# Optimization experiments

Measured on AMD Instinct MI355X. Metric: run time of the kernel, lower is better.

## Reference

```python
import jax, jax.numpy as jnp
import numpy as np

B, L, H, E = 4, 2048, 8, 64
NEG = -1e30  # stand-in for the repo's -3.4e38 overflow-to-inf masking trick


def setup_inputs() -> dict:
    key = jax.random.key(0)
    kq, kk, kv = jax.random.split(key, 3)
    return {
        "queries": jax.random.normal(kq, (B, L, H, E), dtype=jnp.float32),
        "keys": jax.random.normal(kk, (B, L, H, E), dtype=jnp.float32),
        "values": jax.random.normal(kv, (B, L, H, E), dtype=jnp.float32),
    }


def reference(queries, keys, values):
    b, l, h, e = queries.shape
    s = keys.shape[1]
    scale = 1.0 / np.sqrt(e).astype(np.float32)
    # [B,H,L,S] scores, materialized as in the original einsum
    scores = jnp.einsum('blhe,bshe->bhls', queries, keys)
    causal = jnp.tril(jnp.ones((l, s), dtype=bool))  # True = visible
    scores = jnp.where(causal, scores, NEG)
    A = jax.nn.softmax(scale * scores, axis=-1)  # dropout is identity at inference
    return jnp.einsum('bhls,bshd->blhd', A, values)
```

## Files before the change

### kernel.cpp

```cpp
#include <hip/hip_runtime.h>
#include <hip/hip_bf16.h>

namespace {

constexpr int B_ = 4, L = 2048, H = 8, E = 64;
constexpr int RS = H * E;
constexpr float CS = 0.125f * 1.44269504f;
constexpr float THR2 = 11.5f;

constexpr size_t ACCF = (size_t)2 * 32 * 8 * 128 * 64;
constexpr size_t MOFF = ACCF;
constexpr size_t PART_ROWS = (size_t)32 * 8 * 128;
constexpr size_t LOFF = MOFF + 2 * PART_ROWS;
constexpr size_t PART_FLOATS = LOFF + 2 * PART_ROWS;

typedef __attribute__((ext_vector_type(8))) short bf16x8;
typedef __attribute__((ext_vector_type(4))) float f32x4;

__device__ inline unsigned cvt2(float a, float b) {
  __hip_bfloat162 hh = __float22bfloat162_rn(make_float2(a, b));
  union { __hip_bfloat162 h; unsigned u; } c; c.h = hh; return c.u;
}

__global__ __launch_bounds__(512)
void fa_split(const float* __restrict__ Q, const float* __restrict__ K,
              const float* __restrict__ V, float* __restrict__ O,
              float* __restrict__ ws, int splitMode)
{
  const int tid  = (int)threadIdx.x;
  const int lane = tid & 63;
  const int wv   = tid >> 6;
  const int bi   = (int)blockIdx.x;
  const int bh   = bi & 31;
  const int pp   = (bi >> 5) & 7;
  const int role = splitMode ? (bi >> 8) : 2;
  const int b = bh >> 3, h = bh & 7;
  const int ln = lane & 15, lg = lane >> 4, d0 = lg * 4;

  int total, ph1sb0, qgA, k0A, qgB; bool finA, finB; int part;
  const int g = pp, v = 15 - pp;
  if (role == 0)      { total = 17; ph1sb0 = 2*g+2; qgA = g; k0A = 0;        finA = true;  qgB = v; finB = false; part = 0; }
  else if (role == 1) { total = 17; ph1sb0 = 1000;  qgA = v; k0A = 15 - 2*g; finA = false; qgB = 0; finB = false; part = 1; }
  else                { total = 34; ph1sb0 = 2*g+2; qgA = g; k0A = 0;        finA = true;  qgB = v; finB = true;  part = 0; }

  const size_t base = (size_t)b * L * RS + (size_t)h * E;
  const float* Qb = Q + base;
  const float* Kb = K + base;
  const float* Vb = V + base;
  float*       Ob = O + base;

  __shared__ __align__(16) unsigned char KT[2][64 * 128];
  __shared__ __align__(16) unsigned char VT[2][64 * 128];

  const int vdd = tid & 63, vc = tid >> 6;
  const int vkb = 4 * vc + ((vc >> 2) << 4);
  const int kky = tid >> 3, kc = tid & 7;
  float vr[8]; float4 kr0, kr1;

  auto stage_load = [&](int ks) {
    const int kv0 = ks * 64;
    const float* vp = Vb + (size_t)(kv0 + vkb) * RS + vdd;
#pragma unroll
    for (int j = 0; j < 4; ++j) vr[j] = vp[(size_t)j * RS];
#pragma unroll
    for (int j = 0; j < 4; ++j) vr[4 + j] = vp[(size_t)(16 + j) * RS];
    const float* kp = Kb + (size_t)(kv0 + kky) * RS + 8 * kc;
    kr0 = *(const float4*)kp; kr1 = *(const float4*)(kp + 4);
  };
  auto stage_write = [&](int bufI) {
    union { uint4 q; unsigned u[4]; } w;
    w.u[0] = cvt2(vr[0], vr[1]); w.u[1] = cvt2(vr[2], vr[3]);
    w.u[2] = cvt2(vr[4], vr[5]); w.u[3] = cvt2(vr[6], vr[7]);
    *(uint4*)(VT[bufI] + vdd * 128 + 16 * (vc ^ (vdd & 7))) = w.q;
    union { uint4 q; unsigned u[4]; } y;
    y.u[0] = cvt2(kr0.x, kr0.y); y.u[1] = cvt2(kr0.z, kr0.w);
    y.u[2] = cvt2(kr1.x, kr1.y); y.u[3] = cvt2(kr1.z, kr1.w);
    *(uint4*)(KT[bufI] + kky * 128 + 16 * (kc ^ (kky & 7))) = y.q;
  };

  int qg = qgA; bool curFin = finA;
  int qrow0 = qg * 128 + wv * 16;
  int nsW   = (qrow0 + 79) >> 6;

  bf16x8 qf0, qf1;
  auto load_q = [&]() {
    const float* qp = Qb + (size_t)(qrow0 + ln) * RS + 8 * lg;
    float4 a = *(const float4*)qp,        c = *(const float4*)(qp + 4);
    float4 d = *(const float4*)(qp + 32), e = *(const float4*)(qp + 36);
    union { bf16x8 v8; unsigned u[4]; } r0, r1;
    r0.u[0] = cvt2(a.x * CS, a.y * CS); r0.u[1] = cvt2(a.z * CS, a.w * CS);
    r0.u[2] = cvt2(c.x * CS, c.y * CS); r0.u[3] = cvt2(c.z * CS, c.w * CS);
    r1.u[0] = cvt2(d.x * CS, d.y * CS); r1.u[1] = cvt2(d.z * CS, d.w * CS);
    r1.u[2] = cvt2(e.x * CS, e.y * CS); r1.u[3] = cvt2(e.z * CS, e.w * CS);
    qf0 = r0.v8; qf1 = r1.v8;
  };
  load_q();

  f32x4 acc[4];
#pragma unroll
  for (int nt = 0; nt < 4; ++nt) acc[nt] = (f32x4){0.f, 0.f, 0.f, 0.f};
  float m = -1e30f, lsum = 0.f;

  auto epilogue = [&]() {
    float ls = lsum + __shfl_xor(lsum, 16, 64);
    ls += __shfl_xor(ls, 32, 64);
    if (curFin) {
      const float il = 1.0f / ls;
      float inv[4];
#pragma unroll
      for (int r = 0; r < 4; ++r) inv[r] = __shfl(il, d0 + r, 64);
#pragma unroll
      for (int nt = 0; nt < 4; ++nt)
#pragma unroll
        for (int r = 0; r < 4; ++r)
          Ob[(size_t)(qrow0 + d0 + r) * RS + (ln + 16 * nt)] = acc[nt][r] * inv[r];
    } else {
      const int vg = qg - 8;
      const size_t rb = ((size_t)part * 32 + bh) * 1024 + (size_t)vg * 128;
#pragma unroll
      for (int nt = 0; nt < 4; ++nt)
#pragma unroll
        for (int r = 0; r < 4; ++r)
          ws[(rb + wv * 16 + d0 + r) * 64 + ln + 16 * nt] = acc[nt][r];
      if (lane < 16) {
        ws[MOFF + rb + wv * 16 + lane] = m;
        ws[LOFF + rb + wv * 16 + lane] = ls;
      }
    }
  };

  stage_load(k0A);
  stage_write(0);
  __syncthreads();
  int buf = 0;

  for (int sb = 0; sb < total; ++sb) {
    const bool haveNext = (sb + 1) < total;
    if (haveNext) {
      const int sn = sb + 1;
      stage_load((sn < ph1sb0) ? (k0A + sn) : (sn - ph1sb0));
    }
    const int kstep = (sb < ph1sb0) ? (k0A + sb) : (sb - ph1sb0);

    if (kstep < nsW) {
      const unsigned char* Kt = KT[buf];
      const int swzr = 16 * (ln & 7);

      f32x4 st[4];
#pragma unroll
      for (int kt = 0; kt < 4; ++kt) {
        const unsigned char* kr = Kt + (16 * kt + ln) * 128;
        const bf16x8 kfa = *(const bf16x8*)(kr + ((16 * lg) ^ swzr));
        const bf16x8 kfb = *(const bf16x8*)(kr + ((16 * lg + 64) ^ swzr));
        f32x4 s = (f32x4){0.f, 0.f, 0.f, 0.f};
        s = __builtin_amdgcn_mfma_f32_16x16x32_bf16(kfa, qf0, s, 0, 0, 0);
        s = __builtin_amdgcn_mfma_f32_16x16x32_bf16(kfb, qf1, s, 0, 0, 0);
        st[kt] = s;
      }

      float x[16];
#pragma unroll
      for (int kt = 0; kt < 4; ++kt)
#pragma unroll
        for (int r = 0; r < 4; ++r) x[4 * kt + r] = st[kt][r];

      if (kstep == nsW - 1) {
        const int kv0 = kstep * 64;
        const int qr = qrow0 + ln;
#pragma unroll
        for (int kt = 0; kt < 4; ++kt)
#pragma unroll
          for (int r = 0; r < 4; ++r) {
            const int key = kv0 + 16 * kt + d0 + r;
            if (key > qr) x[4 * kt + r] = -1e30f;
          }
      }

      float t8[8];
#pragma unroll
      for (int e = 0; e < 8; ++e) t8[e] = fmaxf(x[e], x[8 + e]);
      float t4a = fmaxf(t8[0], t8[4]), t4b = fmaxf(t8[1], t8[5]);
      float t4c = fmaxf(t8[2], t8[6]), t4d = fmaxf(t8[3], t8[7]);
      float mx = fmaxf(fmaxf(t4a, t4b), fmaxf(t4c, t4d));

      if (!__all(mx <= m + THR2)) {
        float gm = fmaxf(mx, __shfl_xor(mx, 16, 64));
        gm = fmaxf(gm, __shfl_xor(gm, 32, 64));
        const float newm = fmaxf(m, gm);
        const float sc = __builtin_exp2f(m - newm);
        lsum *= sc;
        float scr[4];
#pragma unroll
        for (int r = 0; r < 4; ++r) scr[r] = __shfl(sc, d0 + r, 64);
#pragma unroll
        for (int nt = 0; nt < 4; ++nt) {
          acc[nt][0] *= scr[0]; acc[nt][1] *= scr[1];
          acc[nt][2] *= scr[2]; acc[nt][3] *= scr[3];
        }
        m = newm;
      }

      float p[16];
#pragma unroll
      for (int e = 0; e < 16; ++e) p[e] = __builtin_exp2f(x[e] - m);
      {
        float s8[8];
#pragma unroll
        for (int e = 0; e < 8; ++e) s8[e] = p[e] + p[8 + e];
        float s4a = s8[0] + s8[4], s4b = s8[1] + s8[5];
        float s4c = s8[2] + s8[6], s4d = s8[3] + s8[7];
        lsum += (s4a + s4b) + (s4c + s4d);
      }

      const unsigned char* Vt = VT[buf];
#pragma unroll
      for (int kg = 0; kg < 2; ++kg) {
        union { bf16x8 v8; unsigned u[4]; } pf;
#pragma unroll
        for (int j = 0; j < 4; ++j)
          pf.u[j] = cvt2(p[8 * kg + 2 * j], p[8 * kg + 2 * j + 1]);
#pragma unroll
        for (int nt = 0; nt < 4; ++nt) {
          const int row = ln + 16 * nt;
          const bf16x8 vf = *(const bf16x8*)(
              Vt + row * 128 + 16 * ((lg + 4 * kg) ^ (ln & 7)));
          acc[nt] = __builtin_amdgcn_mfma_f32_16x16x32_bf16(pf.v8, vf, acc[nt], 0, 0, 0);
        }
      }
    }

    if (sb == ph1sb0 - 1) {
      epilogue();
#pragma unroll
      for (int nt = 0; nt < 4; ++nt) acc[nt] = (f32x4){0.f, 0.f, 0.f, 0.f};
      m = -1e30f; lsum = 0.f;
      qg = qgB; curFin = finB;
      qrow0 = qg * 128 + wv * 16;
      nsW = (qrow0 + 79) >> 6;
      load_q();
    }

    if (haveNext) stage_write(buf ^ 1);
    __syncthreads();
    buf ^= 1;
  }

  epilogue();
}

__global__ __launch_bounds__(256)
void fa_merge(const float* __restrict__ ws, float* __restrict__ O)
{
  const int idx = (int)blockIdx.x * 256 + (int)threadIdx.x;
  const int d4  = idx & 15;
  const int row = (idx >> 4) & 127;
  const int vg  = (idx >> 11) & 7;
  const int bh  = idx >> 14;
  const size_t rbase = ((size_t)bh * 8 + vg) * 128 + row;

  const float m0 = ws[MOFF + rbase],             l0 = ws[LOFF + rbase];
  const float m1 = ws[MOFF + PART_ROWS + rbase], l1 = ws[LOFF + PART_ROWS + rbase];
  const float M  = fmaxf(m0, m1);
  const float e0 = __builtin_exp2f(m0 - M), e1 = __builtin_exp2f(m1 - M);
  const float inv = 1.0f / (l0 * e0 + l1 * e1);

  const float4 a0 = *(const float4*)(ws + rbase * 64 + 4 * d4);
  const float4 a1 = *(const float4*)(ws + PART_ROWS * 64 + rbase * 64 + 4 * d4);

  const int b = bh >> 3, h = bh & 7;
  const int orow = (8 + vg) * 128 + row;
  float4 o;
  o.x = (a0.x * e0 + a1.x * e1) * inv;
  o.y = (a0.y * e0 + a1.y * e1) * inv;
  o.z = (a0.z * e0 + a1.z * e1) * inv;
  o.w = (a0.w * e0 + a1.w * e1) * inv;
  *(float4*)(O + ((size_t)(b * L + orow) * H + h) * E + 4 * d4) = o;
}

}

extern "C" void kernel_launch(void* const* d_in, const int* in_sizes, int n_in,
                              void* d_out, int out_size, void* d_ws, size_t ws_size,
                              hipStream_t stream) {
  const float* Q = (const float*)d_in[0];
  const float* K = (const float*)d_in[1];
  const float* V = (const float*)d_in[2];
  float* O = (float*)d_out;
  (void)in_sizes; (void)n_in; (void)out_size;

  const bool split = ws_size >= PART_FLOATS * sizeof(float);
  if (split) {
    fa_split<<<512, 512, 0, stream>>>(Q, K, V, O, (float*)d_ws, 1);
    fa_merge<<<2048, 256, 0, stream>>>((const float*)d_ws, O);
  } else {
    fa_split<<<256, 512, 0, stream>>>(Q, K, V, O, (float*)d_ws, 0);
  }
}
```

Measured before the change: 53.14 us.

## Split causal attention work into finer KV chunks with bf16 partial accumulators

Replaces the two-phase paired-query-group schedule with 1024 blocks, each handling a single query group over a KV range. Heavy groups are split into three or four KV chunks, so each block does about the same amount of work on the 256 CUs. Partial accumulators are stored as bf16 in the MFMA fragment layout to halve workspace traffic, and a table-driven merge kernel combines two or three partials per group. This costs an extra bf16 rounding of partial outputs and more merge work and launches.

```diff
diff --git a/kernel.cpp b/kernel.cpp
--- a/kernel.cpp
+++ b/kernel.cpp
@@ -8,11 +8,11 @@
 constexpr float CS = 0.125f * 1.44269504f;
 constexpr float THR2 = 11.5f;
 
-constexpr size_t ACCF = (size_t)2 * 32 * 8 * 128 * 64;
-constexpr size_t MOFF = ACCF;
-constexpr size_t PART_ROWS = (size_t)32 * 8 * 128;
-constexpr size_t LOFF = MOFF + 2 * PART_ROWS;
-constexpr size_t PART_FLOATS = LOFF + 2 * PART_ROWS;
+constexpr size_t ACC_UINTS = (size_t)4 * 32 * 8 * 4096;
+constexpr size_t MOFF = ACC_UINTS;
+constexpr size_t MCNT = (size_t)4 * 32 * 8 * 128;
+constexpr size_t LOFF = MOFF + MCNT;
+constexpr size_t WS_FLOATS = LOFF + MCNT;
 
 typedef __attribute__((ext_vector_type(8))) short bf16x8;
 typedef __attribute__((ext_vector_type(4))) float f32x4;
@@ -20,6 +20,9 @@
 __device__ inline unsigned cvt2(float a, float b) {
   __hip_bfloat162 hh = __float22bfloat162_rn(make_float2(a, b));
   union { __hip_bfloat162 h; unsigned u; } c; c.h = hh; return c.u;
+}
+__device__ inline float bf2f(unsigned short u) {
+  union { unsigned u; float f; } c; c.u = (unsigned)u << 16; return c.f;
 }
 
 __global__ __launch_bounds__(512)
@@ -33,15 +36,36 @@
   const int bi   = (int)blockIdx.x;
   const int bh   = bi & 31;
   const int pp   = (bi >> 5) & 7;
-  const int role = splitMode ? (bi >> 8) : 2;
+  const int role = bi >> 8;
   const int b = bh >> 3, h = bh & 7;
   const int ln = lane & 15, lg = lane >> 4, d0 = lg * 4;
 
-  int total, ph1sb0, qgA, k0A, qgB; bool finA, finB; int part;
   const int g = pp, v = 15 - pp;
-  if (role == 0)      { total = 17; ph1sb0 = 2*g+2; qgA = g; k0A = 0;        finA = true;  qgB = v; finB = false; part = 0; }
-  else if (role == 1) { total = 17; ph1sb0 = 1000;  qgA = v; k0A = 15 - 2*g; finA = false; qgB = 0; finB = false; part = 1; }
-  else                { total = 34; ph1sb0 = 2*g+2; qgA = g; k0A = 0;        finA = true;  qgB = v; finB = true;  part = 0; }
+  const int b0 = 2 * g + 2, nsv = 32 - 2 * g;
+
+  int grp, kLo, kHi, slot = -1; bool fin = false;
+  if (splitMode) {
+    if (g <= 4) {
+      if (role == 0) { grp = g; kLo = 0; kHi = b0; fin = true; }
+      else {
+        const int c1 = (nsv + 2) / 3, c2 = c1 + (nsv - c1 + 1) / 2;
+        grp = v; slot = role;
+        if (role == 1)      { kLo = 0;  kHi = c1; }
+        else if (role == 2) { kLo = c1; kHi = c2; }
+        else                { kLo = c2; kHi = nsv; }
+      }
+    } else {
+      const int hh = b0 / 2, hv = nsv / 2;
+      if (role == 0)      { grp = g; kLo = 0;  kHi = hh;  slot = 0; }
+      else if (role == 1) { grp = g; kLo = hh; kHi = b0;  slot = 1; }
+      else if (role == 2) { grp = v; kLo = 0;  kHi = hv;  slot = 2; }
+      else                { grp = v; kLo = hv; kHi = nsv; slot = 3; }
+    }
+  } else {
+    if (role == 0) { grp = g; kLo = 0; kHi = b0; }
+    else           { grp = v; kLo = 0; kHi = nsv; }
+    fin = true;
+  }
 
   const size_t base = (size_t)b * L * RS + (size_t)h * E;
   const float* Qb = Q + base;
@@ -78,12 +102,11 @@
     *(uint4*)(KT[bufI] + kky * 128 + 16 * (kc ^ (kky & 7))) = y.q;
   };
 
-  int qg = qgA; bool curFin = finA;
-  int qrow0 = qg * 128 + wv * 16;
-  int nsW   = (qrow0 + 79) >> 6;
+  const int qrow0 = grp * 128 + wv * 16;
+  const int nsW   = (qrow0 + 79) >> 6;
 
   bf16x8 qf0, qf1;
-  auto load_q = [&]() {
+  {
     const float* qp = Qb + (size_t)(qrow0 + ln) * RS + 8 * lg;
     float4 a = *(const float4*)qp,        c = *(const float4*)(qp + 4);
     float4 d = *(const float4*)(qp + 32), e = *(const float4*)(qp + 36);
@@ -93,56 +116,23 @@
     r1.u[0] = cvt2(d.x * CS, d.y * CS); r1.u[1] = cvt2(d.z * CS, d.w * CS);
     r1.u[2] = cvt2(e.x * CS, e.y * CS); r1.u[3] = cvt2(e.z * CS, e.w * CS);
     qf0 = r0.v8; qf1 = r1.v8;
-  };
-  load_q();
+  }
 
   f32x4 acc[4];
 #pragma unroll
   for (int nt = 0; nt < 4; ++nt) acc[nt] = (f32x4){0.f, 0.f, 0.f, 0.f};
   float m = -1e30f, lsum = 0.f;
 
-  auto epilogue = [&]() {
-    float ls = lsum + __shfl_xor(lsum, 16, 64);
-    ls += __shfl_xor(ls, 32, 64);
-    if (curFin) {
-      const float il = 1.0f / ls;
-      float inv[4];
-#pragma unroll
-      for (int r = 0; r < 4; ++r) inv[r] = __shfl(il, d0 + r, 64);
-#pragma unroll
-      for (int nt = 0; nt < 4; ++nt)
-#pragma unroll
-        for (int r = 0; r < 4; ++r)
-          Ob[(size_t)(qrow0 + d0 + r) * RS + (ln + 16 * nt)] = acc[nt][r] * inv[r];
-    } else {
-      const int vg = qg - 8;
-      const size_t rb = ((size_t)part * 32 + bh) * 1024 + (size_t)vg * 128;
-#pragma unroll
-      for (int nt = 0; nt < 4; ++nt)
-#pragma unroll
-        for (int r = 0; r < 4; ++r)
-          ws[(rb + wv * 16 + d0 + r) * 64 + ln + 16 * nt] = acc[nt][r];
-      if (lane < 16) {
-        ws[MOFF + rb + wv * 16 + lane] = m;
-        ws[LOFF + rb + wv * 16 + lane] = ls;
-      }
-    }
-  };
-
-  stage_load(k0A);
+  stage_load(kLo);
   stage_write(0);
   __syncthreads();
   int buf = 0;
 
-  for (int sb = 0; sb < total; ++sb) {
-    const bool haveNext = (sb + 1) < total;
-    if (haveNext) {
-      const int sn = sb + 1;
-      stage_load((sn < ph1sb0) ? (k0A + sn) : (sn - ph1sb0));
-    }
-    const int kstep = (sb < ph1sb0) ? (k0A + sb) : (sb - ph1sb0);
-
-    if (kstep < nsW) {
+  for (int ks = kLo; ks < kHi; ++ks) {
+    const bool haveNext = (ks + 1) < kHi;
+    if (haveNext) stage_load(ks + 1);
+
+    if (ks < nsW) {
       const unsigned char* Kt = KT[buf];
       const int swzr = 16 * (ln & 7);
 
@@ -164,8 +154,8 @@
 #pragma unroll
         for (int r = 0; r < 4; ++r) x[4 * kt + r] = st[kt][r];
 
-      if (kstep == nsW - 1) {
-        const int kv0 = kstep * 64;
+      if (ks == nsW - 1) {
+        const int kv0 = ks * 64;
         const int qr = qrow0 + ln;
 #pragma unroll
         for (int kt = 0; kt < 4; ++kt)
@@ -229,52 +219,103 @@
       }
     }
 
-    if (sb == ph1sb0 - 1) {
-      epilogue();
-#pragma unroll
-      for (int nt = 0; nt < 4; ++nt) acc[nt] = (f32x4){0.f, 0.f, 0.f, 0.f};
-      m = -1e30f; lsum = 0.f;
-      qg = qgB; curFin = finB;
-      qrow0 = qg * 128 + wv * 16;
-      nsW = (qrow0 + 79) >> 6;
-      load_q();
-    }
-
     if (haveNext) stage_write(buf ^ 1);
     __syncthreads();
     buf ^= 1;
   }
 
-  epilogue();
+  float ls = lsum + __shfl_xor(lsum, 16, 64);
+  ls += __shfl_xor(ls, 32, 64);
+  if (fin) {
+    const float il = 1.0f / ls;
+    float inv[4];
+#pragma unroll
+    for (int r = 0; r < 4; ++r) inv[r] = __shfl(il, d0 + r, 64);
+#pragma unroll
+    for (int nt = 0; nt < 4; ++nt)
+#pragma unroll
+      for (int r = 0; r < 4; ++r)
+        Ob[(size_t)(qrow0 + d0 + r) * RS + (ln + 16 * nt)] = acc[nt][r] * inv[r];
+  } else {
+    unsigned* wsu = (unsigned*)ws;
+    const size_t ubase =
+        ((((size_t)slot * 32 + bh) * 8 + pp) * 8 + wv) * 512 + (size_t)lane * 8;
+    uint4 u0, u1;
+    u0.x = cvt2(acc[0][0], acc[0][1]); u0.y = cvt2(acc[0][2], acc[0][3]);
+    u0.z = cvt2(acc[1][0], acc[1][1]); u0.w = cvt2(acc[1][2], acc[1][3]);
+    u1.x = cvt2(acc[2][0], acc[2][1]); u1.y = cvt2(acc[2][2], acc[2][3]);
+    u1.z = cvt2(acc[3][0], acc[3][1]); u1.w = cvt2(acc[3][2], acc[3][3]);
+    *(uint4*)(wsu + ubase)     = u0;
+    *(uint4*)(wsu + ubase + 4) = u1;
+    if (lane < 16) {
+      const size_t mi = (((size_t)slot * 32 + bh) * 8 + pp) * 128 + wv * 16 + lane;
+      ws[MOFF + mi] = m;
+      ws[LOFF + mi] = ls;
+    }
+  }
 }
 
 __global__ __launch_bounds__(256)
 void fa_merge(const float* __restrict__ ws, float* __restrict__ O)
 {
-  const int idx = (int)blockIdx.x * 256 + (int)threadIdx.x;
-  const int d4  = idx & 15;
-  const int row = (idx >> 4) & 127;
-  const int vg  = (idx >> 11) & 7;
-  const int bh  = idx >> 14;
-  const size_t rbase = ((size_t)bh * 8 + vg) * 128 + row;
-
-  const float m0 = ws[MOFF + rbase],             l0 = ws[LOFF + rbase];
-  const float m1 = ws[MOFF + PART_ROWS + rbase], l1 = ws[LOFF + PART_ROWS + rbase];
-  const float M  = fmaxf(m0, m1);
-  const float e0 = __builtin_exp2f(m0 - M), e1 = __builtin_exp2f(m1 - M);
-  const float inv = 1.0f / (l0 * e0 + l1 * e1);
-
-  const float4 a0 = *(const float4*)(ws + rbase * 64 + 4 * d4);
-  const float4 a1 = *(const float4*)(ws + PART_ROWS * 64 + rbase * 64 + 4 * d4);
+  const int bi  = (int)blockIdx.x;
+  const int sub = bi & 7;
+  const int pr  = bi >> 3;
+  const int gi  = pr >> 5, bh = pr & 31;
+  const int tid = (int)threadIdx.x;
+  const int d4  = tid & 15;
+  const int row = sub * 16 + (tid >> 4);
+
+  const int Gt[11] = {5,6,7, 8,9,10, 11,12,13,14,15};
+  const int nS[11] = {2,2,2, 2,2,2, 3,3,3,3,3};
+  const int S0[11] = {0,0,0, 2,2,2, 1,1,1,1,1};
+  const int S1[11] = {1,1,1, 3,3,3, 2,2,2,2,2};
+  const int S2[11] = {0,0,0, 0,0,0, 3,3,3,3,3};
+
+  const int G  = Gt[gi];
+  const int n  = nS[gi];
+  const int pp = (G <= 7) ? G : (15 - G);
+  int sl[3] = {S0[gi], S1[gi], S2[gi]};
+
+  float mv[3], lv[3];
+#pragma unroll
+  for (int i = 0; i < 3; ++i) {
+    if (i < n) {
+      const size_t mi = (((size_t)sl[i] * 32 + bh) * 8 + pp) * 128 + row;
+      mv[i] = ws[MOFF + mi]; lv[i] = ws[LOFF + mi];
+    } else { mv[i] = -1e30f; lv[i] = 0.f; }
+  }
+  float M = fmaxf(mv[0], mv[1]); if (n > 2) M = fmaxf(M, mv[2]);
+  float w[3]; float den = 0.f;
+#pragma unroll
+  for (int i = 0; i < 3; ++i) {
+    w[i] = (i < n) ? __builtin_exp2f(mv[i] - M) : 0.f;
+    den += lv[i] * w[i];
+  }
+  const float inv = 1.0f / den;
+
+  const int wvq = row >> 4, lgq = (row & 15) >> 2, r = row & 3;
+  const int rp = r >> 1, rlo = r & 1;
+  const unsigned short* wsh = (const unsigned short*)ws;
+  float o[4] = {0.f, 0.f, 0.f, 0.f};
+#pragma unroll
+  for (int i = 0; i < 3; ++i) {
+    if (i >= n) break;
+    const size_t base_u =
+        ((((size_t)sl[i] * 32 + bh) * 8 + pp) * 8 + wvq) * 512;
+#pragma unroll
+    for (int j = 0; j < 4; ++j) {
+      const int dim = 4 * d4 + j;
+      const int ln = dim & 15, nt = dim >> 4;
+      const size_t ua = base_u + (size_t)(lgq * 16 + ln) * 8 + nt * 2 + rp;
+      o[j] += bf2f(wsh[ua * 2 + rlo]) * w[i];
+    }
+  }
 
   const int b = bh >> 3, h = bh & 7;
-  const int orow = (8 + vg) * 128 + row;
-  float4 o;
-  o.x = (a0.x * e0 + a1.x * e1) * inv;
-  o.y = (a0.y * e0 + a1.y * e1) * inv;
-  o.z = (a0.z * e0 + a1.z * e1) * inv;
-  o.w = (a0.w * e0 + a1.w * e1) * inv;
-  *(float4*)(O + ((size_t)(b * L + orow) * H + h) * E + 4 * d4) = o;
+  const size_t off = ((size_t)(b * L + G * 128 + row) * H + h) * E + 4 * d4;
+  float4 ov; ov.x = o[0] * inv; ov.y = o[1] * inv; ov.z = o[2] * inv; ov.w = o[3] * inv;
+  *(float4*)(O + off) = ov;
 }
 
 }
@@ -288,11 +329,11 @@
   float* O = (float*)d_out;
   (void)in_sizes; (void)n_in; (void)out_size;
 
-  const bool split = ws_size >= PART_FLOATS * sizeof(float);
+  const bool split = ws_size >= WS_FLOATS * sizeof(float);
   if (split) {
-    fa_split<<<512, 512, 0, stream>>>(Q, K, V, O, (float*)d_ws, 1);
-    fa_merge<<<2048, 256, 0, stream>>>((const float*)d_ws, O);
+    fa_split<<<1024, 512, 0, stream>>>(Q, K, V, O, (float*)d_ws, 1);
+    fa_merge<<<2816, 256, 0, stream>>>((const float*)d_ws, O);
   } else {
-    fa_split<<<256, 512, 0, stream>>>(Q, K, V, O, (float*)d_ws, 0);
-  }
-}
+    fa_split<<<512, 512, 0, stream>>>(Q, K, V, O, (float*)d_ws, 0);
+  }
+}
```

Measured after the change: 64.30 us. +21.0%, slower.

## Switch to 32x32x16 MFMA with 32-row waves and 256-row query groups

Applied to the files above, without the earlier changes.

Replaces the 16x16x32 bf16 MFMA tiles with 32x32x16 tiles so each wave handles 32 query rows, and makes each block cover 256 query rows, halving the grid. The split schedule is rebuilt around 8 query groups, with 18 steps per role. P is rearranged into the MFMA A-operand layout using v_permlane32_swap, avoiding a trip through LDS. This aims to reuse K/V tiles loaded into LDS across more rows and to issue fewer MFMA instructions, at the cost of higher register pressure and only 256 blocks on a chip with 256 CUs, which may leave occupancy low.

```diff
diff --git a/kernel.cpp b/kernel.cpp
--- a/kernel.cpp
+++ b/kernel.cpp
@@ -14,8 +14,8 @@
 constexpr size_t LOFF = MOFF + 2 * PART_ROWS;
 constexpr size_t PART_FLOATS = LOFF + 2 * PART_ROWS;
 
-typedef __attribute__((ext_vector_type(8))) short bf16x8;
-typedef __attribute__((ext_vector_type(4))) float f32x4;
+typedef __attribute__((ext_vector_type(8)))  short bf16x8;
+typedef __attribute__((ext_vector_type(16))) float f32x16;
 
 __device__ inline unsigned cvt2(float a, float b) {
   __hip_bfloat162 hh = __float22bfloat162_rn(make_float2(a, b));
@@ -32,16 +32,22 @@
   const int wv   = tid >> 6;
   const int bi   = (int)blockIdx.x;
   const int bh   = bi & 31;
-  const int pp   = (bi >> 5) & 7;
-  const int role = splitMode ? (bi >> 8) : 2;
+  const int pq   = (bi >> 5) & 3;
+  const int role = splitMode ? (bi >> 7) : 0;
   const int b = bh >> 3, h = bh & 7;
-  const int ln = lane & 15, lg = lane >> 4, d0 = lg * 4;
-
-  int total, ph1sb0, qgA, k0A, qgB; bool finA, finB; int part;
-  const int g = pp, v = 15 - pp;
-  if (role == 0)      { total = 17; ph1sb0 = 2*g+2; qgA = g; k0A = 0;        finA = true;  qgB = v; finB = false; part = 0; }
-  else if (role == 1) { total = 17; ph1sb0 = 1000;  qgA = v; k0A = 15 - 2*g; finA = false; qgB = 0; finB = false; part = 1; }
-  else                { total = 34; ph1sb0 = 2*g+2; qgA = g; k0A = 0;        finA = true;  qgB = v; finB = true;  part = 0; }
+  const int ln32 = lane & 31, hb = lane >> 5;
+  const int rsw  = ln32 & 7;
+
+  const int g = pq, v = 7 - pq;
+  const int ng = 4 * g + 4;
+
+  int total, ph1, grpA, k0A, grpB; bool finA, finB; int part;
+  if (splitMode) {
+    if (role == 0) { total = 18; ph1 = ng;   grpA = g; k0A = 0;       finA = true;  grpB = v; finB = false; part = 0; }
+    else           { total = 18; ph1 = 1000; grpA = v; k0A = 18 - ng; finA = false; grpB = 0; finB = false; part = 1; }
+  } else {
+    total = 36; ph1 = ng; grpA = g; k0A = 0; finA = true; grpB = v; finB = true; part = 0;
+  }
 
   const size_t base = (size_t)b * L * RS + (size_t)h * E;
   const float* Qb = Q + base;
@@ -53,17 +59,14 @@
   __shared__ __align__(16) unsigned char VT[2][64 * 128];
 
   const int vdd = tid & 63, vc = tid >> 6;
-  const int vkb = 4 * vc + ((vc >> 2) << 4);
   const int kky = tid >> 3, kc = tid & 7;
   float vr[8]; float4 kr0, kr1;
 
   auto stage_load = [&](int ks) {
     const int kv0 = ks * 64;
-    const float* vp = Vb + (size_t)(kv0 + vkb) * RS + vdd;
-#pragma unroll
-    for (int j = 0; j < 4; ++j) vr[j] = vp[(size_t)j * RS];
-#pragma unroll
-    for (int j = 0; j < 4; ++j) vr[4 + j] = vp[(size_t)(16 + j) * RS];
+    const float* vp = Vb + (size_t)(kv0 + 8 * vc) * RS + vdd;
+#pragma unroll
+    for (int j = 0; j < 8; ++j) vr[j] = vp[(size_t)j * RS];
     const float* kp = Kb + (size_t)(kv0 + kky) * RS + 8 * kc;
     kr0 = *(const float4*)kp; kr1 = *(const float4*)(kp + 4);
   };
@@ -78,53 +81,54 @@
     *(uint4*)(KT[bufI] + kky * 128 + 16 * (kc ^ (kky & 7))) = y.q;
   };
 
-  int qg = qgA; bool curFin = finA;
-  int qrow0 = qg * 128 + wv * 16;
-  int nsW   = (qrow0 + 79) >> 6;
-
-  bf16x8 qf0, qf1;
+  int grp = grpA; bool curFin = finA;
+  int qrow0 = grp * 256 + wv * 32;
+  int nsW   = 4 * grp + 1 + (wv >> 1);
+
+  bf16x8 qf[4];
   auto load_q = [&]() {
-    const float* qp = Qb + (size_t)(qrow0 + ln) * RS + 8 * lg;
-    float4 a = *(const float4*)qp,        c = *(const float4*)(qp + 4);
-    float4 d = *(const float4*)(qp + 32), e = *(const float4*)(qp + 36);
-    union { bf16x8 v8; unsigned u[4]; } r0, r1;
-    r0.u[0] = cvt2(a.x * CS, a.y * CS); r0.u[1] = cvt2(a.z * CS, a.w * CS);
-    r0.u[2] = cvt2(c.x * CS, c.y * CS); r0.u[3] = cvt2(c.z * CS, c.w * CS);
-    r1.u[0] = cvt2(d.x * CS, d.y * CS); r1.u[1] = cvt2(d.z * CS, d.w * CS);
-    r1.u[2] = cvt2(e.x * CS, e.y * CS); r1.u[3] = cvt2(e.z * CS, e.w * CS);
-    qf0 = r0.v8; qf1 = r1.v8;
+    const float* qp = Qb + (size_t)(qrow0 + ln32) * RS + 8 * hb;
+#pragma unroll
+    for (int ds = 0; ds < 4; ++ds) {
+      float4 a = *(const float4*)(qp + 16 * ds);
+      float4 c = *(const float4*)(qp + 16 * ds + 4);
+      union { bf16x8 v8; unsigned u[4]; } r;
+      r.u[0] = cvt2(a.x * CS, a.y * CS); r.u[1] = cvt2(a.z * CS, a.w * CS);
+      r.u[2] = cvt2(c.x * CS, c.y * CS); r.u[3] = cvt2(c.z * CS, c.w * CS);
+      qf[ds] = r.v8;
+    }
   };
   load_q();
 
-  f32x4 acc[4];
-#pragma unroll
-  for (int nt = 0; nt < 4; ++nt) acc[nt] = (f32x4){0.f, 0.f, 0.f, 0.f};
+  f32x16 zero;
+#pragma unroll
+  for (int i = 0; i < 16; ++i) zero[i] = 0.f;
+  f32x16 accA = zero, accB = zero;
   float m = -1e30f, lsum = 0.f;
 
   auto epilogue = [&]() {
-    float ls = lsum + __shfl_xor(lsum, 16, 64);
-    ls += __shfl_xor(ls, 32, 64);
+    float ls = lsum + __shfl_xor(lsum, 32, 64);
     if (curFin) {
       const float il = 1.0f / ls;
-      float inv[4];
-#pragma unroll
-      for (int r = 0; r < 4; ++r) inv[r] = __shfl(il, d0 + r, 64);
-#pragma unroll
-      for (int nt = 0; nt < 4; ++nt)
-#pragma unroll
-        for (int r = 0; r < 4; ++r)
-          Ob[(size_t)(qrow0 + d0 + r) * RS + (ln + 16 * nt)] = acc[nt][r] * inv[r];
+#pragma unroll
+      for (int r2 = 0; r2 < 16; ++r2) {
+        const int row = (r2 & 3) + 8 * (r2 >> 2) + 4 * hb;
+        const float inv = __shfl(il, row, 64);
+        Ob[(size_t)(qrow0 + row) * RS + ln32]      = accA[r2] * inv;
+        Ob[(size_t)(qrow0 + row) * RS + 32 + ln32] = accB[r2] * inv;
+      }
     } else {
-      const int vg = qg - 8;
-      const size_t rb = ((size_t)part * 32 + bh) * 1024 + (size_t)vg * 128;
-#pragma unroll
-      for (int nt = 0; nt < 4; ++nt)
-#pragma unroll
-        for (int r = 0; r < 4; ++r)
-          ws[(rb + wv * 16 + d0 + r) * 64 + ln + 16 * nt] = acc[nt][r];
-      if (lane < 16) {
-        ws[MOFF + rb + wv * 16 + lane] = m;
-        ws[LOFF + rb + wv * 16 + lane] = ls;
+      const size_t rb = ((size_t)part * 32 + bh) * 1024 + (size_t)(grp - 4) * 256;
+#pragma unroll
+      for (int r2 = 0; r2 < 16; ++r2) {
+        const int row = (r2 & 3) + 8 * (r2 >> 2) + 4 * hb;
+        const size_t lr = rb + wv * 32 + row;
+        ws[lr * 64 + ln32]      = accA[r2];
+        ws[lr * 64 + 32 + ln32] = accB[r2];
+      }
+      if (lane < 32) {
+        ws[MOFF + rb + wv * 32 + lane] = m;
+        ws[LOFF + rb + wv * 32 + lane] = ls;
       }
     }
   };
@@ -138,105 +142,109 @@
     const bool haveNext = (sb + 1) < total;
     if (haveNext) {
       const int sn = sb + 1;
-      stage_load((sn < ph1sb0) ? (k0A + sn) : (sn - ph1sb0));
-    }
-    const int kstep = (sb < ph1sb0) ? (k0A + sb) : (sb - ph1sb0);
+      stage_load((sn < ph1) ? (k0A + sn) : (sn - ph1));
+    }
+    const int kstep = (sb < ph1) ? (k0A + sb) : (sb - ph1);
 
     if (kstep < nsW) {
       const unsigned char* Kt = KT[buf];
-      const int swzr = 16 * (ln & 7);
-
-      f32x4 st[4];
-#pragma unroll
-      for (int kt = 0; kt < 4; ++kt) {
-        const unsigned char* kr = Kt + (16 * kt + ln) * 128;
-        const bf16x8 kfa = *(const bf16x8*)(kr + ((16 * lg) ^ swzr));
-        const bf16x8 kfb = *(const bf16x8*)(kr + ((16 * lg + 64) ^ swzr));
-        f32x4 s = (f32x4){0.f, 0.f, 0.f, 0.f};
-        s = __builtin_amdgcn_mfma_f32_16x16x32_bf16(kfa, qf0, s, 0, 0, 0);
-        s = __builtin_amdgcn_mfma_f32_16x16x32_bf16(kfb, qf1, s, 0, 0, 0);
-        st[kt] = s;
-      }
-
-      float x[16];
-#pragma unroll
-      for (int kt = 0; kt < 4; ++kt)
-#pragma unroll
-        for (int r = 0; r < 4; ++r) x[4 * kt + r] = st[kt][r];
+
+      f32x16 st0 = zero, st1 = zero;
+#pragma unroll
+      for (int ds = 0; ds < 4; ++ds) {
+        const int ch = 16 * ((2 * ds + hb) ^ rsw);
+        const bf16x8 kf0 = *(const bf16x8*)(Kt + ln32 * 128 + ch);
+        const bf16x8 kf1 = *(const bf16x8*)(Kt + (32 + ln32) * 128 + ch);
+        st0 = __builtin_amdgcn_mfma_f32_32x32x16_bf16(kf0, qf[ds], st0, 0, 0, 0);
+        st1 = __builtin_amdgcn_mfma_f32_32x32x16_bf16(kf1, qf[ds], st1, 0, 0, 0);
+      }
+
+      float x[32];
+#pragma unroll
+      for (int r2 = 0; r2 < 16; ++r2) { x[r2] = st0[r2]; x[16 + r2] = st1[r2]; }
 
       if (kstep == nsW - 1) {
         const int kv0 = kstep * 64;
-        const int qr = qrow0 + ln;
-#pragma unroll
-        for (int kt = 0; kt < 4; ++kt)
-#pragma unroll
-          for (int r = 0; r < 4; ++r) {
-            const int key = kv0 + 16 * kt + d0 + r;
-            if (key > qr) x[4 * kt + r] = -1e30f;
-          }
-      }
-
+        const int qr = qrow0 + ln32;
+#pragma unroll
+        for (int e = 0; e < 32; ++e) {
+          const int key = kv0 + 32 * (e >> 4) + 8 * ((e >> 2) & 3) + (e & 3) + 4 * hb;
+          if (key > qr) x[e] = -1e30f;
+        }
+      }
+
+      float t16[16];
+#pragma unroll
+      for (int e = 0; e < 16; ++e) t16[e] = fmaxf(x[e], x[16 + e]);
       float t8[8];
 #pragma unroll
-      for (int e = 0; e < 8; ++e) t8[e] = fmaxf(x[e], x[8 + e]);
+      for (int e = 0; e < 8; ++e) t8[e] = fmaxf(t16[e], t16[8 + e]);
       float t4a = fmaxf(t8[0], t8[4]), t4b = fmaxf(t8[1], t8[5]);
       float t4c = fmaxf(t8[2], t8[6]), t4d = fmaxf(t8[3], t8[7]);
-      float mx = fmaxf(fmaxf(t4a, t4b), fmaxf(t4c, t4d));
+      const float mx = fmaxf(fmaxf(t4a, t4b), fmaxf(t4c, t4d));
 
       if (!__all(mx <= m + THR2)) {
-        float gm = fmaxf(mx, __shfl_xor(mx, 16, 64));
-        gm = fmaxf(gm, __shfl_xor(gm, 32, 64));
+        float gm = fmaxf(mx, __shfl_xor(mx, 32, 64));
         const float newm = fmaxf(m, gm);
         const float sc = __builtin_exp2f(m - newm);
         lsum *= sc;
-        float scr[4];
-#pragma unroll
-        for (int r = 0; r < 4; ++r) scr[r] = __shfl(sc, d0 + r, 64);
-#pragma unroll
-        for (int nt = 0; nt < 4; ++nt) {
-          acc[nt][0] *= scr[0]; acc[nt][1] *= scr[1];
-          acc[nt][2] *= scr[2]; acc[nt][3] *= scr[3];
+        float scr[16];
+#pragma unroll
+        for (int r2 = 0; r2 < 16; ++r2) {
+          const int row = (r2 & 3) + 8 * (r2 >> 2) + 4 * hb;
+          scr[r2] = __shfl(sc, row, 64);
         }
+#pragma unroll
+        for (int r2 = 0; r2 < 16; ++r2) { accA[r2] *= scr[r2]; accB[r2] *= scr[r2]; }
         m = newm;
       }
 
-      float p[16];
-#pragma unroll
-      for (int e = 0; e < 16; ++e) p[e] = __builtin_exp2f(x[e] - m);
+      float p[32];
+#pragma unroll
+      for (int e = 0; e < 32; ++e) p[e] = __builtin_exp2f(x[e] - m);
       {
+        float s16[16];
+#pragma unroll
+        for (int e = 0; e < 16; ++e) s16[e] = p[e] + p[16 + e];
         float s8[8];
 #pragma unroll
-        for (int e = 0; e < 8; ++e) s8[e] = p[e] + p[8 + e];
-        float s4a = s8[0] + s8[4], s4b = s8[1] + s8[5];
-        float s4c = s8[2] + s8[6], s4d = s8[3] + s8[7];
-        lsum += (s4a + s4b) + (s4c + s4d);
+        for (int e = 0; e < 8; ++e) s8[e] = s16[e] + s16[8 + e];
+        const float sa = (s8[0] + s8[4]) + (s8[1] + s8[5]);
+        const float sb2 = (s8[2] + s8[6]) + (s8[3] + s8[7]);
+        lsum += sa + sb2;
       }
 
       const unsigned char* Vt = VT[buf];
 #pragma unroll
-      for (int kg = 0; kg < 2; ++kg) {
-        union { bf16x8 v8; unsigned u[4]; } pf;
-#pragma unroll
-        for (int j = 0; j < 4; ++j)
-          pf.u[j] = cvt2(p[8 * kg + 2 * j], p[8 * kg + 2 * j + 1]);
-#pragma unroll
-        for (int nt = 0; nt < 4; ++nt) {
-          const int row = ln + 16 * nt;
-          const bf16x8 vf = *(const bf16x8*)(
-              Vt + row * 128 + 16 * ((lg + 4 * kg) ^ (ln & 7)));
-          acc[nt] = __builtin_amdgcn_mfma_f32_16x16x32_bf16(pf.v8, vf, acc[nt], 0, 0, 0);
+      for (int kt = 0; kt < 2; ++kt) {
+#pragma unroll
+        for (int hh2 = 0; hh2 < 2; ++hh2) {
+          const int ks = 2 * kt + hh2;
+          const int pb = 16 * kt + 8 * hh2;
+          unsigned w0 = cvt2(p[pb + 0], p[pb + 1]);
+          unsigned w2 = cvt2(p[pb + 4], p[pb + 5]);
+          asm("v_permlane32_swap_b32 %0, %1" : "+v"(w0), "+v"(w2));
+          unsigned w1 = cvt2(p[pb + 2], p[pb + 3]);
+          unsigned w3 = cvt2(p[pb + 6], p[pb + 7]);
+          asm("v_permlane32_swap_b32 %0, %1" : "+v"(w1), "+v"(w3));
+          union { bf16x8 v8; unsigned u[4]; } A;
+          A.u[0] = w0; A.u[1] = w1; A.u[2] = w2; A.u[3] = w3;
+          const int chv = 16 * ((2 * ks + hb) ^ rsw);
+          const bf16x8 vf0 = *(const bf16x8*)(Vt + ln32 * 128 + chv);
+          const bf16x8 vf1 = *(const bf16x8*)(Vt + (32 + ln32) * 128 + chv);
+          accA = __builtin_amdgcn_mfma_f32_32x32x16_bf16(A.v8, vf0, accA, 0, 0, 0);
+          accB = __builtin_amdgcn_mfma_f32_32x32x16_bf16(A.v8, vf1, accB, 0, 0, 0);
         }
       }
     }
 
-    if (sb == ph1sb0 - 1) {
+    if (sb == ph1 - 1) {
       epilogue();
-#pragma unroll
-      for (int nt = 0; nt < 4; ++nt) acc[nt] = (f32x4){0.f, 0.f, 0.f, 0.f};
+      accA = zero; accB = zero;
       m = -1e30f; lsum = 0.f;
-      qg = qgB; curFin = finB;
-      qrow0 = qg * 128 + wv * 16;
-      nsW = (qrow0 + 79) >> 6;
+      grp = grpB; curFin = finB;
+      qrow0 = grp * 256 + wv * 32;
+      nsW = 4 * grp + 1 + (wv >> 1);
       load_q();
     }
 
@@ -290,9 +298,9 @@
 
   const bool split = ws_size >= PART_FLOATS * sizeof(float);
   if (split) {
-    fa_split<<<512, 512, 0, stream>>>(Q, K, V, O, (float*)d_ws, 1);
+    fa_split<<<256, 512, 0, stream>>>(Q, K, V, O, (float*)d_ws, 1);
     fa_merge<<<2048, 256, 0, stream>>>((const float*)d_ws, O);
   } else {
-    fa_split<<<256, 512, 0, stream>>>(Q, K, V, O, (float*)d_ws, 0);
+    fa_split<<<128, 512, 0, stream>>>(Q, K, V, O, (float*)d_ws, 0);
   }
 }
```

Measured after the change: 60.53 us. 1.14x slower.
